# Kernel tuning notes

Hardware: AMD Instinct MI355X
Metric: run time of the kernel (lower is better)

Reference implementation:

```python
import jax, jax.numpy as jnp
import numpy as np

B, U, D, N, O = 128, 16, 256, 1024, 256
RES_CONN, IN_CONN, BIAS_P = 0.2, 0.2, 0.5


def _fixed_bernoulli(rng, heads, rows, cols, conn):
    # each column has exactly nb = int(conn*rows) ones (as in the torch code)
    nb = max(1, int(conn * rows))
    r = rng.random((heads, rows, cols))
    thr = np.sort(r, axis=1)[:, nb - 1:nb, :]
    return (r <= thr).astype(np.float32)


def setup_inputs() -> dict:
    rng = np.random.default_rng(0)
    # recurrent weights: normal * fixed-bernoulli mask, normalized by spectral radius
    W = rng.normal(size=(U, N, N)).astype(np.float32) * _fixed_bernoulli(rng, U, N, N, RES_CONN)
    sr0 = np.abs(np.linalg.eigvals(W.astype(np.float64))).max(axis=-1).astype(np.float32).reshape(U, 1, 1)
    W = W / sr0
    Win = _fixed_bernoulli(rng, U, D, N, IN_CONN)
    bias = (rng.random((U, 1, N)) < BIAS_P).astype(np.float32)
    Wout = rng.normal(size=(U, N, O)).astype(np.float32)
    adaptive_lr = rng.random((U, D, 1)).astype(np.float32)
    sr = rng.random((U, 1, 1)).astype(np.float32)
    temperature = np.ones((1,), np.float32)
    X = rng.normal(size=(B, U, D)).astype(np.float32)
    state = rng.normal(size=(B, U, N)).astype(np.float32)
    arrs = dict(X=X, state=state, W=W, Win=Win, bias=bias, Wout=Wout,
                sr=sr, adaptive_lr=adaptive_lr, temperature=temperature)
    return {k: jnp.asarray(v) for k, v in arrs.items()}


def reference(X, state, W, Win, bias, Wout, sr, adaptive_lr, temperature):
    # X: [B,U,D] -> [B,U,1,D]; state: [B,U,N] -> [B,U,1,N]
    x = X[:, :, None, :]
    s = state[:, :, None, :]
    # adaptive per-unit learning rate: softmax over the units axis
    lr = jax.nn.softmax(jnp.einsum('buid,udk->buik', x, adaptive_lr) / temperature, axis=1)  # [B,U,1,1]
    feed = jnp.einsum('buid,udn->buin', x, Win)            # [B,U,1,N]
    echo = jnp.einsum('buin,unm->buim', s, W * sr) + bias  # [B,U,1,N]
    new_state = (1.0 - lr) * s + lr * jnp.tanh(feed + echo)
    output = jnp.einsum('buin,uno->buio', new_state, Wout)  # [B,U,1,O]
    return new_state[:, :, 0, :], output[:, :, 0, :]
```

## Files before the change

### kernel.cpp

```cpp
#include <hip/hip_runtime.h>
#include <math.h>

#define Bsz 128
#define Usz 16
#define Dsz 256
#define Nsz 1024
#define Osz 256
#define BK  64
#define LDT 72

typedef __attribute__((ext_vector_type(2))) unsigned int u32x2;
typedef __attribute__((ext_vector_type(4))) unsigned int u32x4;
typedef __attribute__((ext_vector_type(4))) float f32x4;
typedef __attribute__((ext_vector_type(8))) short bf16x8;

__device__ __forceinline__ unsigned int fbits(float f) {
    union { float f; unsigned int u; } v; v.f = f; return v.u;
}
__device__ __forceinline__ unsigned int pk(float lo, float hi) {
    return __builtin_amdgcn_perm(fbits(hi), fbits(lo), 0x07060302u);
}
__device__ __forceinline__ unsigned short bf16t(float f) {
    return (unsigned short)(fbits(f) >> 16);
}

__device__ __forceinline__ void sync_nodrain() {
    __builtin_amdgcn_sched_barrier(0);
    asm volatile("s_waitcnt lgkmcnt(0)");
    __builtin_amdgcn_sched_barrier(0);
    __builtin_amdgcn_s_barrier();
    __builtin_amdgcn_sched_barrier(0);
}

__global__ __launch_bounds__(256)
void lr_kernel(const float* __restrict__ X, const float* __restrict__ alr,
               const float* __restrict__ temp, float* __restrict__ lr)
{
    const int b = blockIdx.x;
    const int t = threadIdx.x;
    const int u = t >> 4;
    const int l = t & 15;
    const f32x4* xp = (const f32x4*)(X + ((size_t)b * Usz + u) * Dsz + l * 16);
    const f32x4* ap = (const f32x4*)(alr + (size_t)u * Dsz + l * 16);
    float s = 0.f;
    #pragma unroll
    for (int j = 0; j < 4; j++) {
        const f32x4 xv = xp[j], av = ap[j];
        s += xv[0]*av[0] + xv[1]*av[1] + xv[2]*av[2] + xv[3]*av[3];
    }
    s += __shfl_down(s, 8, 16);
    s += __shfl_down(s, 4, 16);
    s += __shfl_down(s, 2, 16);
    s += __shfl_down(s, 1, 16);
    __shared__ float logits[16];
    if (l == 0) logits[u] = s;
    __syncthreads();
    if (t < 16) {
        const float T = temp[0];
        float m = -1e30f;
        #pragma unroll
        for (int i = 0; i < 16; i++) m = fmaxf(m, logits[i] / T);
        float sum = 0.f;
        #pragma unroll
        for (int i = 0; i < 16; i++) sum += expf(logits[i] / T - m);
        lr[(size_t)b * Usz + t] = expf(logits[t] / T - m) / sum;
    }
}

__global__ __launch_bounds__(256)
void state_gemm(const float* __restrict__ X, const float* __restrict__ state,
                const float* __restrict__ W, const float* __restrict__ Win,
                const float* __restrict__ bias, const float* __restrict__ sr,
                const float* __restrict__ lr, float* __restrict__ out0)
{
    const int id = blockIdx.x;
    const int nt = id & 31;
    const int u  = (id >> 5) & 15;
    const int mt = id >> 9;

    const int tid  = threadIdx.x;
    const int wave = tid >> 6, lane = tid & 63;
    const int l16  = lane & 15, kgl = lane >> 4;
    const int wm = wave & 1, wn = wave >> 1;

    __shared__ unsigned short As[2][64 * LDT];
    __shared__ unsigned short Bs[2][32 * LDT];

    const float sru = sr[u];

    const int rA = tid >> 2;
    const int cA = (tid & 3) * 16;
    const int kB = tid >> 3;
    const int nB = (tid & 7) * 4;
    const int col0 = nt * 32;

    f32x4 rAE[4], rAO[4];
    f32x4 rBE[2], rBO[2];

    auto ldA = [&](int s, f32x4 (&ra)[4]) {
        const int k0 = s * BK;
        const float* base = (k0 < Dsz)
            ? X     + (((size_t)(mt * 64 + rA) * Usz + u) * Dsz) + k0 + cA
            : state + (((size_t)(mt * 64 + rA) * Usz + u) * Nsz) + (k0 - Dsz) + cA;
        #pragma unroll
        for (int j = 0; j < 4; j++) ra[j] = *(const f32x4*)(base + 4 * j);
    };
    auto ldB = [&](int s, f32x4 (&rb)[2]) {
        const int k0 = s * BK;
        const float* base = (k0 < Dsz)
            ? Win + (size_t)u * Dsz * Nsz + (size_t)(k0 + kB) * Nsz + col0 + nB
            : W   + (size_t)u * Nsz * Nsz + (size_t)(k0 - Dsz + kB) * Nsz + col0 + nB;
        rb[0] = *(const f32x4*)base;
        rb[1] = *(const f32x4*)(base + (size_t)32 * Nsz);
    };
    auto wrA = [&](int p, f32x4 (&ra)[4]) {
        #pragma unroll
        for (int j = 0; j < 4; j++) {
            u32x2 w; w[0] = pk(ra[j][0], ra[j][1]); w[1] = pk(ra[j][2], ra[j][3]);
            *(u32x2*)&As[p][rA * LDT + cA + 4 * j] = w;
        }
    };
    auto wrB = [&](int p, f32x4 (&rb)[2], float sc) {
        #pragma unroll
        for (int h = 0; h < 2; h++)
            #pragma unroll
            for (int j = 0; j < 4; j++)
                Bs[p][(nB + j) * LDT + kB + 32 * h] = bf16t(rb[h][j] * sc);
    };

    f32x4 acc[2] = {};
    auto comp = [&](int p) {
        #pragma unroll
        for (int kk = 0; kk < 2; kk++) {
            const bf16x8 bf = *(const bf16x8*)&Bs[p][(wn * 16 + l16) * LDT + kk * 32 + kgl * 8];
            #pragma unroll
            for (int mi = 0; mi < 2; mi++) {
                const bf16x8 af = *(const bf16x8*)&As[p][(wm * 32 + mi * 16 + l16) * LDT + kk * 32 + kgl * 8];
                acc[mi] = __builtin_amdgcn_mfma_f32_16x16x32_bf16(af, bf, acc[mi], 0, 0, 0);
            }
        }
    };
    auto scB = [&](int s) -> float { return (s * BK < Dsz) ? 1.f : sru; };

    ldA(0, rAE); ldB(0, rBE);
    ldA(1, rAO); ldB(1, rBO);
    wrA(0, rAE); wrB(0, rBE, scB(0));
    sync_nodrain();

    for (int s2 = 0; s2 < 10; s2++) {
        const int s = 2 * s2;
        if (s + 2 < 20) { ldA(s + 2, rAE); ldB(s + 2, rBE); }
        wrA(1, rAO); wrB(1, rBO, scB(s + 1));
        comp(0);
        sync_nodrain();
        if (s + 3 < 20) { ldA(s + 3, rAO); ldB(s + 3, rBO); }
        if (s + 2 < 20) { wrA(0, rAE); wrB(0, rBE, scB(s + 2)); }
        comp(1);
        sync_nodrain();
    }

    const int gcol = nt * 32 + wn * 16 + l16;
    const float bi = bias[u * Nsz + gcol];
    #pragma unroll
    for (int mi = 0; mi < 2; mi++) {
        #pragma unroll
        for (int rg = 0; rg < 4; rg++) {
            const int grow = mt * 64 + wm * 32 + mi * 16 + kgl * 4 + rg;
            const size_t idx = ((size_t)grow * Usz + u) * Nsz + gcol;
            const float th = tanhf(acc[mi][rg] + bi);
            const float lv = lr[grow * Usz + u];
            out0[idx] = (1.f - lv) * state[idx] + lv * th;
        }
    }
}

__global__ __launch_bounds__(256)
void out_gemm(const float* __restrict__ ns, const float* __restrict__ Wout,
              float* __restrict__ dst, int nsteps, int partial)
{
    const int id = blockIdx.x;
    const int ot = id & 7;
    const int u  = (id >> 3) & 15;
    const int mt = (id >> 7) & 1;
    const int ks = id >> 8;
    const int kbase = ks * nsteps * BK;

    const int tid  = threadIdx.x;
    const int wave = tid >> 6, lane = tid & 63;
    const int l16  = lane & 15, kgl = lane >> 4;
    const int wm = wave & 1, wn = wave >> 1;

    __shared__ unsigned short As[2][64 * LDT];
    __shared__ unsigned short Bs[2][32 * LDT];

    const int rA = tid >> 2;
    const int cA = (tid & 3) * 16;
    const int kB = tid >> 3;
    const int nB = (tid & 7) * 4;
    const int col0 = ot * 32;

    f32x4 rAE[4], rAO[4];
    f32x4 rBE[2], rBO[2];

    auto ldA = [&](int s, f32x4 (&ra)[4]) {
        const float* base = ns + (((size_t)(mt * 64 + rA) * Usz + u) * Nsz) + kbase + s * BK + cA;
        #pragma unroll
        for (int j = 0; j < 4; j++) ra[j] = *(const f32x4*)(base + 4 * j);
    };
    auto ldB = [&](int s, f32x4 (&rb)[2]) {
        const float* base = Wout + (size_t)u * Nsz * Osz
                          + (size_t)(kbase + s * BK + kB) * Osz + col0 + nB;
        rb[0] = *(const f32x4*)base;
        rb[1] = *(const f32x4*)(base + (size_t)32 * Osz);
    };
    auto wrA = [&](int p, f32x4 (&ra)[4]) {
        #pragma unroll
        for (int j = 0; j < 4; j++) {
            u32x2 w; w[0] = pk(ra[j][0], ra[j][1]); w[1] = pk(ra[j][2], ra[j][3]);
            *(u32x2*)&As[p][rA * LDT + cA + 4 * j] = w;
        }
    };
    auto wrB = [&](int p, f32x4 (&rb)[2]) {
        #pragma unroll
        for (int h = 0; h < 2; h++)
            #pragma unroll
            for (int j = 0; j < 4; j++)
                Bs[p][(nB + j) * LDT + kB + 32 * h] = bf16t(rb[h][j]);
    };

    f32x4 acc[2] = {};
    auto comp = [&](int p) {
        #pragma unroll
        for (int kk = 0; kk < 2; kk++) {
            const bf16x8 bf = *(const bf16x8*)&Bs[p][(wn * 16 + l16) * LDT + kk * 32 + kgl * 8];
            #pragma unroll
            for (int mi = 0; mi < 2; mi++) {
                const bf16x8 af = *(const bf16x8*)&As[p][(wm * 32 + mi * 16 + l16) * LDT + kk * 32 + kgl * 8];
                acc[mi] = __builtin_amdgcn_mfma_f32_16x16x32_bf16(af, bf, acc[mi], 0, 0, 0);
            }
        }
    };

    ldA(0, rAE); ldB(0, rBE);
    ldA(1, rAO); ldB(1, rBO);
    wrA(0, rAE); wrB(0, rBE);
    sync_nodrain();

    for (int s2 = 0; s2 < nsteps / 2; s2++) {
        const int s = 2 * s2;
        if (s + 2 < nsteps) { ldA(s + 2, rAE); ldB(s + 2, rBE); }
        wrA(1, rAO); wrB(1, rBO);
        comp(0);
        sync_nodrain();
        if (s + 3 < nsteps) { ldA(s + 3, rAO); ldB(s + 3, rBO); }
        if (s + 2 < nsteps) { wrA(0, rAE); wrB(0, rBE); }
        comp(1);
        sync_nodrain();
    }

    const int gcol = ot * 32 + wn * 16 + l16;
    #pragma unroll
    for (int mi = 0; mi < 2; mi++) {
        #pragma unroll
        for (int rg = 0; rg < 4; rg++) {
            const int grow = mt * 64 + wm * 32 + mi * 16 + kgl * 4 + rg;
            if (partial)
                dst[(((size_t)ks * 16 + u) * 128 + grow) * 256 + gcol] = acc[mi][rg];
            else
                dst[((size_t)grow * Usz + u) * Osz + gcol] = acc[mi][rg];
        }
    }
}

__global__ __launch_bounds__(256)
void out_reduce(const float* __restrict__ part, float* __restrict__ out1)
{
    const size_t i = (size_t)blockIdx.x * 256 + threadIdx.x;
    const size_t base = i * 4;
    const int m = (int)(base >> 12);
    const int u = (int)((base >> 8) & 15);
    const int o = (int)(base & 255);

    const size_t pb = ((size_t)u * 128 + m) * 256 + o;
    const size_t slab = (size_t)16 * 128 * 256;
    f32x4 s = *(const f32x4*)(part + pb);
    s += *(const f32x4*)(part + pb + slab);
    s += *(const f32x4*)(part + pb + 2 * slab);
    s += *(const f32x4*)(part + pb + 3 * slab);
    *(f32x4*)(out1 + base) = s;
}

extern "C" void kernel_launch(void* const* d_in, const int* in_sizes, int n_in,
                              void* d_out, int out_size, void* d_ws, size_t ws_size,
                              hipStream_t stream)
{
    (void)in_sizes; (void)n_in; (void)out_size;
    const float* X     = (const float*)d_in[0];
    const float* state = (const float*)d_in[1];
    const float* W     = (const float*)d_in[2];
    const float* Win   = (const float*)d_in[3];
    const float* bias  = (const float*)d_in[4];
    const float* Wout  = (const float*)d_in[5];
    const float* sr    = (const float*)d_in[6];
    const float* alr   = (const float*)d_in[7];
    const float* temp  = (const float*)d_in[8];

    float* out0 = (float*)d_out;
    float* out1 = out0 + (size_t)Bsz * Usz * Nsz;
    float* lr   = (float*)d_ws;

    const size_t p_off   = 8192;
    const size_t p_bytes = (size_t)4 * 16 * 128 * 256 * 4;

    lr_kernel<<<Bsz, 256, 0, stream>>>(X, alr, temp, lr);
    state_gemm<<<1024, 256, 0, stream>>>(X, state, W, Win, bias, sr, lr, out0);

    if (ws_size >= p_off + p_bytes) {
        float* part = (float*)((char*)d_ws + p_off);
        out_gemm<<<1024, 256, 0, stream>>>(out0, Wout, part, 4, 1);
        out_reduce<<<512, 256, 0, stream>>>(part, out1);
    } else {
        out_gemm<<<256, 256, 0, stream>>>(out0, Wout, out1, 16, 0);
    }
}
```

Before: 194.2 us.

## Cover full batch per block with 512 threads and swizzle B tile in LDS

Both GEMM kernels now use 512-thread blocks that cover all 128 batch rows instead of two 64-row tiles. Each weight tile is therefore loaded from global memory once rather than twice, and each thread loads one B vector instead of two. The B tile in LDS now uses an XOR swizzle on the k-groups to reduce bank conflicts on the scalar transposed writes, and A writes use wider 128-bit stores. The trade-off is half as many blocks, larger LDS use per block and possibly lower occupancy.

```diff
diff --git a/kernel.cpp b/kernel.cpp
--- a/kernel.cpp
+++ b/kernel.cpp
@@ -67,72 +67,79 @@
     }
 }
 
-__global__ __launch_bounds__(256)
+__global__ __launch_bounds__(512)
 void state_gemm(const float* __restrict__ X, const float* __restrict__ state,
                 const float* __restrict__ W, const float* __restrict__ Win,
                 const float* __restrict__ bias, const float* __restrict__ sr,
                 const float* __restrict__ lr, float* __restrict__ out0)
 {
     const int id = blockIdx.x;
-    const int nt = id & 31;
-    const int u  = (id >> 5) & 15;
-    const int mt = id >> 9;
+    const int u  = id & 15;
+    const int nt = id >> 4;
 
     const int tid  = threadIdx.x;
-    const int wave = tid >> 6, lane = tid & 63;
+    const int wave = tid >> 6;
+    const int lane = tid & 63;
     const int l16  = lane & 15, kgl = lane >> 4;
-    const int wm = wave & 1, wn = wave >> 1;
-
-    __shared__ unsigned short As[2][64 * LDT];
+    const int wm = wave & 3, wn = wave >> 2;
+
+    __shared__ unsigned short As[2][128 * LDT];
     __shared__ unsigned short Bs[2][32 * LDT];
 
     const float sru = sr[u];
+    const int col0 = nt * 32;
 
     const int rA = tid >> 2;
     const int cA = (tid & 3) * 16;
     const int kB = tid >> 3;
     const int nB = (tid & 7) * 4;
-    const int col0 = nt * 32;
+    const int gB = kB >> 3, kL = kB & 7;
 
     f32x4 rAE[4], rAO[4];
-    f32x4 rBE[2], rBO[2];
+    f32x4 rBE,    rBO;
 
     auto ldA = [&](int s, f32x4 (&ra)[4]) {
         const int k0 = s * BK;
         const float* base = (k0 < Dsz)
-            ? X     + (((size_t)(mt * 64 + rA) * Usz + u) * Dsz) + k0 + cA
-            : state + (((size_t)(mt * 64 + rA) * Usz + u) * Nsz) + (k0 - Dsz) + cA;
+            ? X     + ((size_t)rA * Usz + u) * Dsz + k0 + cA
+            : state + ((size_t)rA * Usz + u) * Nsz + (k0 - Dsz) + cA;
         #pragma unroll
         for (int j = 0; j < 4; j++) ra[j] = *(const f32x4*)(base + 4 * j);
     };
-    auto ldB = [&](int s, f32x4 (&rb)[2]) {
+    auto ldB = [&](int s, f32x4& rb) {
         const int k0 = s * BK;
         const float* base = (k0 < Dsz)
             ? Win + (size_t)u * Dsz * Nsz + (size_t)(k0 + kB) * Nsz + col0 + nB
             : W   + (size_t)u * Nsz * Nsz + (size_t)(k0 - Dsz + kB) * Nsz + col0 + nB;
-        rb[0] = *(const f32x4*)base;
-        rb[1] = *(const f32x4*)(base + (size_t)32 * Nsz);
+        rb = *(const f32x4*)base;
     };
     auto wrA = [&](int p, f32x4 (&ra)[4]) {
-        #pragma unroll
-        for (int j = 0; j < 4; j++) {
-            u32x2 w; w[0] = pk(ra[j][0], ra[j][1]); w[1] = pk(ra[j][2], ra[j][3]);
-            *(u32x2*)&As[p][rA * LDT + cA + 4 * j] = w;
-        }
-    };
-    auto wrB = [&](int p, f32x4 (&rb)[2], float sc) {
-        #pragma unroll
-        for (int h = 0; h < 2; h++)
-            #pragma unroll
-            for (int j = 0; j < 4; j++)
-                Bs[p][(nB + j) * LDT + kB + 32 * h] = bf16t(rb[h][j] * sc);
+        u32x4 w0, w1;
+        w0[0] = pk(ra[0][0], ra[0][1]); w0[1] = pk(ra[0][2], ra[0][3]);
+        w0[2] = pk(ra[1][0], ra[1][1]); w0[3] = pk(ra[1][2], ra[1][3]);
+        w1[0] = pk(ra[2][0], ra[2][1]); w1[1] = pk(ra[2][2], ra[2][3]);
+        w1[2] = pk(ra[3][0], ra[3][1]); w1[3] = pk(ra[3][2], ra[3][3]);
+        *(u32x4*)&As[p][rA * LDT + cA]     = w0;
+        *(u32x4*)&As[p][rA * LDT + cA + 8] = w1;
+    };
+    auto wrB = [&](int p, f32x4& rb, float sc) {
+        const int c = tid & 7;
+        const int go = ((gB ^ c) << 3) + kL;
+        #pragma unroll
+        for (int e = 0; e < 4; e++)
+            Bs[p][(nB + e) * LDT + go] = bf16t(rb[e] * sc);
+    };
+    auto rdB = [&](int p, int kk) -> bf16x8 {
+        const int n = wn * 16 + l16;
+        const int go = (((kk * 4 + kgl) ^ (n >> 2)) << 3);
+        return *(const bf16x8*)&Bs[p][n * LDT + go];
     };
 
     f32x4 acc[2] = {};
     auto comp = [&](int p) {
         #pragma unroll
         for (int kk = 0; kk < 2; kk++) {
-            const bf16x8 bf = *(const bf16x8*)&Bs[p][(wn * 16 + l16) * LDT + kk * 32 + kgl * 8];
+            const bf16x8 bf = rdB(p, kk);
             #pragma unroll
             for (int mi = 0; mi < 2; mi++) {
                 const bf16x8 af = *(const bf16x8*)&As[p][(wm * 32 + mi * 16 + l16) * LDT + kk * 32 + kgl * 8];
@@ -159,13 +166,13 @@
         sync_nodrain();
     }
 
-    const int gcol = nt * 32 + wn * 16 + l16;
+    const int gcol = col0 + wn * 16 + l16;
     const float bi = bias[u * Nsz + gcol];
     #pragma unroll
     for (int mi = 0; mi < 2; mi++) {
         #pragma unroll
         for (int rg = 0; rg < 4; rg++) {
-            const int grow = mt * 64 + wm * 32 + mi * 16 + kgl * 4 + rg;
+            const int grow = wm * 32 + mi * 16 + kgl * 4 + rg;
             const size_t idx = ((size_t)grow * Usz + u) * Nsz + gcol;
             const float th = tanhf(acc[mi][rg] + bi);
             const float lv = lr[grow * Usz + u];
@@ -174,65 +181,71 @@
     }
 }
 
-__global__ __launch_bounds__(256)
+__global__ __launch_bounds__(512)
 void out_gemm(const float* __restrict__ ns, const float* __restrict__ Wout,
               float* __restrict__ dst, int nsteps, int partial)
 {
     const int id = blockIdx.x;
     const int ot = id & 7;
     const int u  = (id >> 3) & 15;
-    const int mt = (id >> 7) & 1;
-    const int ks = id >> 8;
+    const int ks = id >> 7;
     const int kbase = ks * nsteps * BK;
 
     const int tid  = threadIdx.x;
-    const int wave = tid >> 6, lane = tid & 63;
+    const int wave = tid >> 6;
+    const int lane = tid & 63;
     const int l16  = lane & 15, kgl = lane >> 4;
-    const int wm = wave & 1, wn = wave >> 1;
-
-    __shared__ unsigned short As[2][64 * LDT];
+    const int wm = wave & 3, wn = wave >> 2;
+
+    __shared__ unsigned short As[2][128 * LDT];
     __shared__ unsigned short Bs[2][32 * LDT];
 
+    const int col0 = ot * 32;
     const int rA = tid >> 2;
     const int cA = (tid & 3) * 16;
     const int kB = tid >> 3;
     const int nB = (tid & 7) * 4;
-    const int col0 = ot * 32;
+    const int gB = kB >> 3, kL = kB & 7;
 
     f32x4 rAE[4], rAO[4];
-    f32x4 rBE[2], rBO[2];
+    f32x4 rBE,    rBO;
 
     auto ldA = [&](int s, f32x4 (&ra)[4]) {
-        const float* base = ns + (((size_t)(mt * 64 + rA) * Usz + u) * Nsz) + kbase + s * BK + cA;
+        const float* base = ns + ((size_t)rA * Usz + u) * Nsz + kbase + s * BK + cA;
         #pragma unroll
         for (int j = 0; j < 4; j++) ra[j] = *(const f32x4*)(base + 4 * j);
     };
-    auto ldB = [&](int s, f32x4 (&rb)[2]) {
-        const float* base = Wout + (size_t)u * Nsz * Osz
-                          + (size_t)(kbase + s * BK + kB) * Osz + col0 + nB;
-        rb[0] = *(const f32x4*)base;
-        rb[1] = *(const f32x4*)(base + (size_t)32 * Osz);
+    auto ldB = [&](int s, f32x4& rb) {
+        rb = *(const f32x4*)(Wout + (size_t)u * Nsz * Osz
+                             + (size_t)(kbase + s * BK + kB) * Osz + col0 + nB);
     };
     auto wrA = [&](int p, f32x4 (&ra)[4]) {
-        #pragma unroll
-        for (int j = 0; j < 4; j++) {
-            u32x2 w; w[0] = pk(ra[j][0], ra[j][1]); w[1] = pk(ra[j][2], ra[j][3]);
-            *(u32x2*)&As[p][rA * LDT + cA + 4 * j] = w;
-        }
-    };
-    auto wrB = [&](int p, f32x4 (&rb)[2]) {
-        #pragma unroll
-        for (int h = 0; h < 2; h++)
-            #pragma unroll
-            for (int j = 0; j < 4; j++)
-                Bs[p][(nB + j) * LDT + kB + 32 * h] = bf16t(rb[h][j]);
+        u32x4 w0, w1;
+        w0[0] = pk(ra[0][0], ra[0][1]); w0[1] = pk(ra[0][2], ra[0][3]);
+        w0[2] = pk(ra[1][0], ra[1][1]); w0[3] = pk(ra[1][2], ra[1][3]);
+        w1[0] = pk(ra[2][0], ra[2][1]); w1[1] = pk(ra[2][2], ra[2][3]);
+        w1[2] = pk(ra[3][0], ra[3][1]); w1[3] = pk(ra[3][2], ra[3][3]);
+        *(u32x4*)&As[p][rA * LDT + cA]     = w0;
+        *(u32x4*)&As[p][rA * LDT + cA + 8] = w1;
+    };
+    auto wrB = [&](int p, f32x4& rb) {
+        const int c = tid & 7;
+        const int go = ((gB ^ c) << 3) + kL;
+        #pragma unroll
+        for (int e = 0; e < 4; e++)
+            Bs[p][(nB + e) * LDT + go] = bf16t(rb[e]);
+    };
+    auto rdB = [&](int p, int kk) -> bf16x8 {
+        const int n = wn * 16 + l16;
+        const int go = (((kk * 4 + kgl) ^ (n >> 2)) << 3);
+        return *(const bf16x8*)&Bs[p][n * LDT + go];
     };
 
     f32x4 acc[2] = {};
     auto comp = [&](int p) {
         #pragma unroll
         for (int kk = 0; kk < 2; kk++) {
-            const bf16x8 bf = *(const bf16x8*)&Bs[p][(wn * 16 + l16) * LDT + kk * 32 + kgl * 8];
+            const bf16x8 bf = rdB(p, kk);
             #pragma unroll
             for (int mi = 0; mi < 2; mi++) {
                 const bf16x8 af = *(const bf16x8*)&As[p][(wm * 32 + mi * 16 + l16) * LDT + kk * 32 + kgl * 8];
@@ -258,12 +271,12 @@
         sync_nodrain();
     }
 
-    const int gcol = ot * 32 + wn * 16 + l16;
+    const int gcol = col0 + wn * 16 + l16;
     #pragma unroll
     for (int mi = 0; mi < 2; mi++) {
         #pragma unroll
         for (int rg = 0; rg < 4; rg++) {
-            const int grow = mt * 64 + wm * 32 + mi * 16 + kgl * 4 + rg;
+            const int grow = wm * 32 + mi * 16 + kgl * 4 + rg;
             if (partial)
                 dst[(((size_t)ks * 16 + u) * 128 + grow) * 256 + gcol] = acc[mi][rg];
             else
@@ -313,13 +326,13 @@
     const size_t p_bytes = (size_t)4 * 16 * 128 * 256 * 4;
 
     lr_kernel<<<Bsz, 256, 0, stream>>>(X, alr, temp, lr);
-    state_gemm<<<1024, 256, 0, stream>>>(X, state, W, Win, bias, sr, lr, out0);
+    state_gemm<<<512, 512, 0, stream>>>(X, state, W, Win, bias, sr, lr, out0);
 
     if (ws_size >= p_off + p_bytes) {
         float* part = (float*)((char*)d_ws + p_off);
-        out_gemm<<<1024, 256, 0, stream>>>(out0, Wout, part, 4, 1);
+        out_gemm<<<512, 512, 0, stream>>>(out0, Wout, part, 4, 1);
         out_reduce<<<512, 256, 0, stream>>>(part, out1);
     } else {
-        out_gemm<<<256, 256, 0, stream>>>(out0, Wout, out1, 16, 0);
-    }
-}
+        out_gemm<<<128, 512, 0, stream>>>(out0, Wout, out1, 16, 0);
+    }
+}
```

Result: faster. 185.5 us (-4.5%).
